# Kernel tuning notes

Measured on AMD Instinct MI355X. Metric: run time of the kernel, lower is better.

Reference implementation:

```python
import jax, jax.numpy as jnp
import numpy as np

B, T, J, D = 32, 2048, 256, 256


def setup_inputs() -> dict:
    key = jax.random.key(0)
    k1, k2, k3, k4, k5 = jax.random.split(key, 5)
    U = jax.random.normal(k1, (B, J, D), jnp.float32)
    H = jax.random.normal(k2, (B, T, D), jnp.float32)
    # realistic length-based binary masks (at least half the positions valid)
    u_len = jax.random.randint(k3, (B,), J // 2, J + 1)
    h_len = jax.random.randint(k4, (B,), T // 2, T + 1)
    U_mask = (jnp.arange(J)[None, :] < u_len[:, None]).astype(jnp.float32)
    H_mask = (jnp.arange(T)[None, :] < h_len[:, None]).astype(jnp.float32)
    # similarity_layer = nn.Linear(3*D, 1); bias initialized to 1.0 in __init__
    w = jax.random.normal(k5, (3 * D,), jnp.float32) * 0.02
    bias = jnp.ones((), jnp.float32)
    return {"U": U, "H": H, "U_mask": U_mask, "H_mask": H_mask, "w": w, "bias": bias}


def _masked_softmax(vector, mask):
    # softmax(vector * mask) * mask, renormalized along the softmax axis
    result = jax.nn.softmax(vector * mask, axis=-1) * mask
    return result / (jnp.sum(result, axis=-1, keepdims=True) + 1e-13)


def reference(U, H, U_mask, H_mask, w, bias):
    # Linear on cat([H, U, H*U]) decomposes into three terms; avoids the
    # (B, T, J, 3D) intermediate while computing identical math.
    w_h, w_u, w_hu = w[:D], w[D:2 * D], w[2 * D:]
    S = ((H @ w_h)[:, :, None]                      # (B, T, 1)
         + (U @ w_u)[:, None, :]                    # (B, 1, J)
         + jnp.einsum('btd,bjd->btj', H * w_hu, U)  # (B, T, J)
         + bias)

    # context-to-question attention: masked softmax over J, then bmm with U
    attn = _masked_softmax(S, U_mask[:, None, :])   # (B, T, J)
    c2q = jnp.einsum('btj,bjd->btd', attn, U)       # (B, T, D)

    # question-to-context: replace masked with -1e7, max over J, softmax over T
    um = U_mask[:, None, :]
    masked_sim = S * um + (-10000000.0) * (1.0 - um)
    mb = jnp.max(masked_sim, axis=-1)               # (B, T)
    b = _masked_softmax(mb, H_mask)                 # (B, T)
    q2c = jnp.einsum('bt,btd->bd', b, H)            # (B, D)

    G = jnp.concatenate([H, c2q, H * c2q, H * q2c[:, None, :]], axis=-1)  # (B, T, 4D)
    return (G, c2q, q2c)
```

## Files before the change

### kernel.cpp

```cpp
#include <hip/hip_runtime.h>
#include <hip/hip_bf16.h>

#define BB 32
#define TT 2048
#define JJ 256
#define DD 256

typedef __attribute__((ext_vector_type(4))) float f32x4;
typedef __attribute__((ext_vector_type(8))) short bf16x8;
typedef __attribute__((ext_vector_type(2))) unsigned int u32x2v;

static __device__ __forceinline__ unsigned short f2bf(float x) {
    unsigned u = __builtin_bit_cast(unsigned, x);
    u = (u + 0x7fffu + ((u >> 16) & 1u)) >> 16;
    return (unsigned short)u;
}
static __device__ __forceinline__ unsigned pack2(float a, float b) {
    return (unsigned)f2bf(a) | ((unsigned)f2bf(b) << 16);
}

static __device__ __forceinline__ void stage_slice(
    const unsigned short* __restrict__ Bsrc, char* pool, int buf, int kt, int tid, int wid)
{
    #pragma unroll
    for (int it = 0; it < 4; ++it) {
        int s = it * 256 + tid;
        int row = s >> 2, cp = s & 3;
        int c = cp ^ (row & 3);
        const char* src = (const char*)Bsrc + row * 512 + kt * 64 + c * 16;
        __builtin_amdgcn_global_load_lds(
            (const __attribute__((address_space(1))) unsigned int*)src,
            (__attribute__((address_space(3))) unsigned int*)(pool + (buf << 14) + (it << 12) + (wid << 10)),
            16, 0, 0);
    }
}

__global__ __launch_bounds__(256) void p0_prep(
    const float* __restrict__ U, const float* __restrict__ w,
    unsigned short* __restrict__ Ubf, unsigned short* __restrict__ UbfT,
    float* __restrict__ Uw, float* __restrict__ q2c_out)
{
    const int b = blockIdx.x >> 2, jc = blockIdx.x & 3;
    const int tid = threadIdx.x;
    if (jc == 0) q2c_out[b * 256 + tid] = 0.f;
    __shared__ unsigned short lt[64][258];
    const f32x4* U4 = (const f32x4*)U;
    const f32x4* W4 = (const f32x4*)w;
    for (int it = 0; it < 16; ++it) {
        int fi = it * 256 + tid;
        int lr = fi >> 6, c4 = fi & 63;
        int j = b * 256 + jc * 64 + lr;
        f32x4 u4 = U4[j * 64 + c4];
        unsigned short s0 = f2bf(u4[0]), s1 = f2bf(u4[1]), s2 = f2bf(u4[2]), s3 = f2bf(u4[3]);
        u32x2v pk; pk[0] = (unsigned)s0 | ((unsigned)s1 << 16); pk[1] = (unsigned)s2 | ((unsigned)s3 << 16);
        *(u32x2v*)(Ubf + j * 256 + c4 * 4) = pk;
        lt[lr][c4*4+0] = s0; lt[lr][c4*4+1] = s1; lt[lr][c4*4+2] = s2; lt[lr][c4*4+3] = s3;
        f32x4 wu = W4[64 + c4];
        float p = u4[0]*wu[0] + u4[1]*wu[1] + u4[2]*wu[2] + u4[3]*wu[3];
        #pragma unroll
        for (int o = 32; o; o >>= 1) p += __shfl_xor(p, o);
        if ((tid & 63) == 0) Uw[j] = p;
    }
    __syncthreads();
    for (int it2 = 0; it2 < 64; ++it2) {
        int d = it2 * 4 + (tid >> 6);
        int jl = tid & 63;
        UbfT[(b * 256 + d) * 256 + jc * 64 + jl] = lt[jl][d];
    }
}

__global__ __launch_bounds__(256, 3) void p1_main(
    const float* __restrict__ H, const float* __restrict__ Um,
    const float* __restrict__ w, const float* __restrict__ biasp,
    const unsigned short* __restrict__ Ubf, const unsigned short* __restrict__ UbfT,
    const float* __restrict__ Uw,
    float* __restrict__ mb, float* __restrict__ Gout, float* __restrict__ c2q_out)
{
    const int id = blockIdx.x;
    const int n = ((id & 7) << 7) | (id >> 3);
    const int b = n >> 5, tb = n & 31;
    const int t0 = tb * 64;
    const int tid = threadIdx.x;
    const int wid = tid >> 6, lane = tid & 63, g = lane >> 4, l16 = lane & 15;

    __shared__ __align__(16) char pool[36864];
    __shared__ float uw_lds[256];
    __shared__ float um_lds[256];
    __shared__ float rt_lds[64];

    const f32x4* H4 = (const f32x4*)H;
    const f32x4* W4 = (const f32x4*)w;
    f32x4* G4 = (f32x4*)Gout;
    f32x4* C2Q4 = (f32x4*)c2q_out;
    const float bias = biasp[0];
    const unsigned short* Ubf_b  = Ubf  + (size_t)b * 65536;
    const unsigned short* UbfT_b = UbfT + (size_t)b * 65536;

    uw_lds[tid] = Uw[b * 256 + tid];
    um_lds[tid] = Um[b * 256 + tid];

    for (int it = 0; it < 16; ++it) {
        int fi = it * 256 + tid;
        int lr = fi >> 6, c4 = fi & 63;
        f32x4 h4 = H4[(b * TT + t0 + lr) * 64 + c4];
        f32x4 whu = W4[128 + c4];
        f32x4 wh = W4[c4];
        G4[(b * TT + t0 + lr) * 256 + c4] = h4;
        f32x4 hw = h4 * whu;
        u32x2v pk; pk[0] = pack2(hw[0], hw[1]); pk[1] = pack2(hw[2], hw[3]);
        unsigned off = ((unsigned)(lr * 512 + c4 * 8)) ^ ((unsigned)((lr & 7) << 4));
        *(u32x2v*)(pool + off) = pk;
        float p = h4[0]*wh[0] + h4[1]*wh[1] + h4[2]*wh[2] + h4[3]*wh[3];
        #pragma unroll
        for (int o = 32; o; o >>= 1) p += __shfl_xor(p, o);
        if (lane == 0) rt_lds[lr] = p;
    }
    __syncthreads();

    bf16x8 af[8];
    {
        const int row = wid * 16 + l16;
        #pragma unroll
        for (int kt = 0; kt < 8; ++kt) {
            unsigned off = ((unsigned)(row * 512 + kt * 64 + g * 16)) ^ ((unsigned)((row & 7) << 4));
            af[kt] = *(const bf16x8*)(pool + off);
        }
    }
    __syncthreads();

    f32x4 acc[16];
    #pragma unroll
    for (int nt = 0; nt < 16; ++nt) acc[nt] = (f32x4)(0.0f);
    stage_slice(Ubf_b, pool, 0, 0, tid, wid);
    __syncthreads();
    #pragma unroll
    for (int kt = 0; kt < 8; ++kt) {
        if (kt < 7) stage_slice(Ubf_b, pool, (kt + 1) & 1, kt + 1, tid, wid);
        const char* bufp = pool + ((kt & 1) << 14);
        #pragma unroll
        for (int nt = 0; nt < 16; ++nt) {
            const int row = nt * 16 + l16;
            bf16x8 bfr = *(const bf16x8*)(bufp + row * 64 + ((g ^ (row & 3)) << 4));
            acc[nt] = __builtin_amdgcn_mfma_f32_16x16x32_bf16(af[kt], bfr, acc[nt], 0, 0, 0);
        }
        __syncthreads();
    }

    float rmax[4] = {-3e38f, -3e38f, -3e38f, -3e38f};
    #pragma unroll
    for (int nt = 0; nt < 16; ++nt) {
        float ct = uw_lds[nt * 16 + l16];
        float msk = um_lds[nt * 16 + l16];
        #pragma unroll
        for (int r = 0; r < 4; ++r) {
            float v = acc[nt][r] + ct;
            acc[nt][r] = v;
            if (msk > 0.5f) rmax[r] = fmaxf(rmax[r], v);
        }
    }
    #pragma unroll
    for (int r = 0; r < 4; ++r) {
        #pragma unroll
        for (int o = 1; o < 16; o <<= 1) rmax[r] = fmaxf(rmax[r], __shfl_xor(rmax[r], o));
    }
    float rsum[4] = {0.f, 0.f, 0.f, 0.f};
    #pragma unroll
    for (int nt = 0; nt < 16; ++nt) {
        float msk = um_lds[nt * 16 + l16];
        #pragma unroll
        for (int r = 0; r < 4; ++r) {
            float e = (msk > 0.5f) ? exp2f((acc[nt][r] - rmax[r]) * 1.44269504f) : 0.0f;
            acc[nt][r] = e;
            rsum[r] += e;
        }
    }
    #pragma unroll
    for (int r = 0; r < 4; ++r) {
        #pragma unroll
        for (int o = 1; o < 16; o <<= 1) rsum[r] += __shfl_xor(rsum[r], o);
    }
    if (l16 == 0) {
        #pragma unroll
        for (int r = 0; r < 4; ++r) {
            int lrow = wid * 16 + g * 4 + r;
            mb[b * TT + t0 + lrow] = rmax[r] + rt_lds[lrow] + bias;
        }
    }
    float inv[4];
    #pragma unroll
    for (int r = 0; r < 4; ++r) inv[r] = 1.0f / rsum[r];

    const unsigned wb = (unsigned)wid * 9216u;
    #pragma unroll
    for (int nt = 0; nt < 16; ++nt) {
        int j = nt * 16 + l16;
        unsigned lo = pack2(acc[nt][0] * inv[0], acc[nt][1] * inv[1]);
        unsigned hi = pack2(acc[nt][2] * inv[2], acc[nt][3] * inv[3]);
        char* p = pool + wb + (unsigned)(j * 36) + (unsigned)(g * 8);
        *(unsigned*)(p) = lo;
        *(unsigned*)(p + 4) = hi;
    }
    bf16x8 pa[8];
    #pragma unroll
    for (int kt = 0; kt < 8; ++kt) {
        #pragma unroll
        for (int jj = 0; jj < 8; ++jj) {
            int j = kt * 32 + g * 8 + jj;
            unsigned short pv = *(const unsigned short*)(pool + wb + (unsigned)(j * 36) + (unsigned)(l16 * 2));
            pa[kt][jj] = (short)pv;
        }
    }
    __syncthreads();

    f32x4 acc2[16];
    #pragma unroll
    for (int nt = 0; nt < 16; ++nt) acc2[nt] = (f32x4)(0.0f);
    stage_slice(UbfT_b, pool, 0, 0, tid, wid);
    __syncthreads();
    #pragma unroll
    for (int kt = 0; kt < 8; ++kt) {
        if (kt < 7) stage_slice(UbfT_b, pool, (kt + 1) & 1, kt + 1, tid, wid);
        const char* bufp = pool + ((kt & 1) << 14);
        #pragma unroll
        for (int nt = 0; nt < 16; ++nt) {
            const int row = nt * 16 + l16;
            bf16x8 bfr = *(const bf16x8*)(bufp + row * 64 + ((g ^ (row & 3)) << 4));
            acc2[nt] = __builtin_amdgcn_mfma_f32_16x16x32_bf16(pa[kt], bfr, acc2[nt], 0, 0, 0);
        }
        __syncthreads();
    }

    {
        float* lds_f = (float*)pool;
        const int c_ = lane & 31, rh = lane >> 5;
        #pragma unroll
        for (int half = 0; half < 2; ++half) {
            #pragma unroll
            for (int nt8 = 0; nt8 < 8; ++nt8) {
                int nt = half * 8 + nt8;
                int dcol = nt8 * 16 + l16;
                #pragma unroll
                for (int r = 0; r < 4; ++r) {
                    int row = wid * 16 + g * 4 + r;
                    lds_f[row * 132 + dcol] = acc2[nt][r];
                }
            }
            #pragma unroll
            for (int it3 = 0; it3 < 8; ++it3) {
                int row = wid * 16 + it3 * 2 + rh;
                f32x4 v = *(const f32x4*)&lds_f[row * 132 + c_ * 4];
                int t = t0 + row;
                f32x4 h4 = H4[(b * TT + t) * 64 + half * 32 + c_];
                int gb4 = (b * TT + t) * 256;
                G4[gb4 + 64 + half * 32 + c_] = v;
                G4[gb4 + 128 + half * 32 + c_] = h4 * v;
                C2Q4[(b * TT + t) * 64 + half * 32 + c_] = v;
            }
        }
    }
}

__global__ __launch_bounds__(256) void p2_fused(
    const float* __restrict__ mb, const float* __restrict__ Hm,
    const float* __restrict__ H, float* __restrict__ q2c_out)
{
    const int b = blockIdx.x >> 4, ch = blockIdx.x & 15;
    const int tid = threadIdx.x;
    __shared__ float red[8];
    float mv[8], hm[8];
    float lmax = -3e38f;
    #pragma unroll
    for (int k = 0; k < 8; ++k) {
        int t = k * 256 + tid;
        mv[k] = mb[b * TT + t];
        hm[k] = Hm[b * TT + t];
        if (hm[k] > 0.5f) lmax = fmaxf(lmax, mv[k]);
    }
    #pragma unroll
    for (int o = 32; o; o >>= 1) lmax = fmaxf(lmax, __shfl_xor(lmax, o));
    int wv = tid >> 6;
    if ((tid & 63) == 0) red[wv] = lmax;
    __syncthreads();
    lmax = fmaxf(fmaxf(red[0], red[1]), fmaxf(red[2], red[3]));
    float ls = 0.f;
    #pragma unroll
    for (int k = 0; k < 8; ++k)
        ls += (hm[k] > 0.5f) ? exp2f((mv[k] - lmax) * 1.44269504f) : 0.f;
    #pragma unroll
    for (int o = 32; o; o >>= 1) ls += __shfl_xor(ls, o);
    if ((tid & 63) == 0) red[4 + wv] = ls;
    __syncthreads();
    const float invs = 1.0f / (red[4] + red[5] + red[6] + red[7] + 1e-13f);

    const int tq = tid >> 6, dq = tid & 63;
    const f32x4* H4 = (const f32x4*)H;
    f32x4 a = (f32x4)(0.0f);
    for (int tt = tq; tt < 128; tt += 4) {
        int t = ch * 128 + tt;
        int k = t >> 8;
        (void)k;
        float bm = mb[b * TT + t];
        float hmv = Hm[b * TT + t];
        float bv = (hmv > 0.5f) ? exp2f((bm - lmax) * 1.44269504f) * invs : 0.f;
        a += bv * H4[(b * TT + t) * 64 + dq];
    }
    __shared__ f32x4 red4[4][64];
    red4[tq][dq] = a;
    __syncthreads();
    if (tid < 64) {
        f32x4 s = red4[0][tid] + red4[1][tid] + red4[2][tid] + red4[3][tid];
        #pragma unroll
        for (int c = 0; c < 4; ++c) atomicAdd(&q2c_out[b * 256 + tid * 4 + c], s[c]);
    }
}

__global__ __launch_bounds__(256) void p3_g3(
    const float* __restrict__ H, const float* __restrict__ q2c,
    float* __restrict__ Gout)
{
    int idx = blockIdx.x * 256 + threadIdx.x;
    int rowid = idx >> 6, c4 = idx & 63;
    int b = rowid >> 11;
    const f32x4* H4 = (const f32x4*)H;
    const f32x4* Q4 = (const f32x4*)q2c;
    f32x4* G4 = (f32x4*)Gout;
    f32x4 h4 = H4[idx];
    f32x4 q4 = Q4[b * 64 + c4];
    G4[rowid * 256 + 192 + c4] = h4 * q4;
}

extern "C" void kernel_launch(void* const* d_in, const int* in_sizes, int n_in,
                              void* d_out, int out_size, void* d_ws, size_t ws_size,
                              hipStream_t stream) {
    (void)in_sizes; (void)n_in; (void)out_size; (void)ws_size;
    const float* U    = (const float*)d_in[0];
    const float* H    = (const float*)d_in[1];
    const float* Um   = (const float*)d_in[2];
    const float* Hm   = (const float*)d_in[3];
    const float* w    = (const float*)d_in[4];
    const float* bias = (const float*)d_in[5];

    float* G   = (float*)d_out;
    float* c2q = G + (size_t)BB * TT * 1024;
    float* q2c = c2q + (size_t)BB * TT * 256;

    char* ws = (char*)d_ws;
    unsigned short* Ubf  = (unsigned short*)ws;
    unsigned short* UbfT = (unsigned short*)(ws + (4u << 20));
    float* Uw   = (float*)(ws + (8u << 20));
    float* mb   = (float*)(ws + (8u << 20) + (64u << 10));

    p0_prep<<<dim3(128), dim3(256), 0, stream>>>(U, w, Ubf, UbfT, Uw, q2c);
    p1_main<<<dim3(1024), dim3(256), 0, stream>>>(H, Um, w, bias, Ubf, UbfT, Uw, mb, G, c2q);
    p2_fused<<<dim3(512), dim3(256), 0, stream>>>(mb, Hm, H, q2c);
    p3_g3<<<dim3(16384), dim3(256), 0, stream>>>(H, q2c, G);
}
```

Before: 154.4 us.

## Use nontemporal stores, drop LDS transpose epilogue, batch p3 loads per thread

Output writes to G and c2q now use nontemporal stores so the large write stream bypasses cache retention. The p1 epilogue no longer transposes the MFMA accumulators through LDS and instead writes scalar elements straight from the accumulator layout. That saves the LDS round trip but gives narrower, strided global stores (16 contiguous floats per row group) and scalar H reloads. p3 now processes four vectors per thread with a quarter of the blocks, so more loads are in flight per thread.

New measurement: 187.2 us. 21.2% more time.

```diff
diff --git a/kernel.cpp b/kernel.cpp
--- a/kernel.cpp
+++ b/kernel.cpp
@@ -91,7 +91,6 @@
     const f32x4* H4 = (const f32x4*)H;
     const f32x4* W4 = (const f32x4*)w;
     f32x4* G4 = (f32x4*)Gout;
-    f32x4* C2Q4 = (f32x4*)c2q_out;
     const float bias = biasp[0];
     const unsigned short* Ubf_b  = Ubf  + (size_t)b * 65536;
     const unsigned short* UbfT_b = UbfT + (size_t)b * 65536;
@@ -105,7 +104,7 @@
         f32x4 h4 = H4[(b * TT + t0 + lr) * 64 + c4];
         f32x4 whu = W4[128 + c4];
         f32x4 wh = W4[c4];
-        G4[(b * TT + t0 + lr) * 256 + c4] = h4;
+        __builtin_nontemporal_store(h4, &G4[(b * TT + t0 + lr) * 256 + c4]);
         f32x4 hw = h4 * whu;
         u32x2v pk; pk[0] = pack2(hw[0], hw[1]); pk[1] = pack2(hw[2], hw[3]);
         unsigned off = ((unsigned)(lr * 512 + c4 * 8)) ^ ((unsigned)((lr & 7) << 4));
@@ -230,32 +229,18 @@
         __syncthreads();
     }
 
-    {
-        float* lds_f = (float*)pool;
-        const int c_ = lane & 31, rh = lane >> 5;
-        #pragma unroll
-        for (int half = 0; half < 2; ++half) {
-            #pragma unroll
-            for (int nt8 = 0; nt8 < 8; ++nt8) {
-                int nt = half * 8 + nt8;
-                int dcol = nt8 * 16 + l16;
-                #pragma unroll
-                for (int r = 0; r < 4; ++r) {
-                    int row = wid * 16 + g * 4 + r;
-                    lds_f[row * 132 + dcol] = acc2[nt][r];
-                }
-            }
-            #pragma unroll
-            for (int it3 = 0; it3 < 8; ++it3) {
-                int row = wid * 16 + it3 * 2 + rh;
-                f32x4 v = *(const f32x4*)&lds_f[row * 132 + c_ * 4];
-                int t = t0 + row;
-                f32x4 h4 = H4[(b * TT + t) * 64 + half * 32 + c_];
-                int gb4 = (b * TT + t) * 256;
-                G4[gb4 + 64 + half * 32 + c_] = v;
-                G4[gb4 + 128 + half * 32 + c_] = h4 * v;
-                C2Q4[(b * TT + t) * 64 + half * 32 + c_] = v;
-            }
+    #pragma unroll
+    for (int nt = 0; nt < 16; ++nt) {
+        int d = nt * 16 + l16;
+        #pragma unroll
+        for (int r = 0; r < 4; ++r) {
+            int t = t0 + wid * 16 + g * 4 + r;
+            float c = acc2[nt][r];
+            float h = H[(b * TT + t) * 256 + d];
+            int gbase = (b * TT + t) * 1024;
+            __builtin_nontemporal_store(c, &Gout[gbase + 256 + d]);
+            __builtin_nontemporal_store(h * c, &Gout[gbase + 512 + d]);
+            __builtin_nontemporal_store(c, &c2q_out[(b * TT + t) * 256 + d]);
         }
     }
 }
@@ -297,8 +282,6 @@
     f32x4 a = (f32x4)(0.0f);
     for (int tt = tq; tt < 128; tt += 4) {
         int t = ch * 128 + tt;
-        int k = t >> 8;
-        (void)k;
         float bm = mb[b * TT + t];
         float hmv = Hm[b * TT + t];
         float bv = (hmv > 0.5f) ? exp2f((bm - lmax) * 1.44269504f) * invs : 0.f;
@@ -318,15 +301,24 @@
     const float* __restrict__ H, const float* __restrict__ q2c,
     float* __restrict__ Gout)
 {
-    int idx = blockIdx.x * 256 + threadIdx.x;
-    int rowid = idx >> 6, c4 = idx & 63;
-    int b = rowid >> 11;
+    const int base = blockIdx.x * 1024 + threadIdx.x;
     const f32x4* H4 = (const f32x4*)H;
     const f32x4* Q4 = (const f32x4*)q2c;
     f32x4* G4 = (f32x4*)Gout;
-    f32x4 h4 = H4[idx];
-    f32x4 q4 = Q4[b * 64 + c4];
-    G4[rowid * 256 + 192 + c4] = h4 * q4;
+    f32x4 h[4];
+    int rowid[4], c4[4];
+    #pragma unroll
+    for (int k = 0; k < 4; ++k) {
+        int idx = base + k * 256;
+        rowid[k] = idx >> 6; c4[k] = idx & 63;
+        h[k] = __builtin_nontemporal_load(&H4[idx]);
+    }
+    #pragma unroll
+    for (int k = 0; k < 4; ++k) {
+        int b = rowid[k] >> 11;
+        f32x4 q4 = Q4[b * 64 + c4[k]];
+        __builtin_nontemporal_store(h[k] * q4, &G4[rowid[k] * 256 + 192 + c4[k]]);
+    }
 }
 
 extern "C" void kernel_launch(void* const* d_in, const int* in_sizes, int n_in,
@@ -353,5 +345,5 @@
     p0_prep<<<dim3(128), dim3(256), 0, stream>>>(U, w, Ubf, UbfT, Uw, q2c);
     p1_main<<<dim3(1024), dim3(256), 0, stream>>>(H, Um, w, bias, Ubf, UbfT, Uw, mb, G, c2q);
     p2_fused<<<dim3(512), dim3(256), 0, stream>>>(mb, Hm, H, q2c);
-    p3_g3<<<dim3(16384), dim3(256), 0, stream>>>(H, q2c, G);
-}
+    p3_g3<<<dim3(4096), dim3(256), 0, stream>>>(H, q2c, G);
+}
```

## Change LDS swizzle for B tiles and replace LDS-transpose epilogue with lane shuffles

Applied to the files above, without the earlier changes.

The XOR swizzle for staged U slices now uses (row>>1)&3 instead of row&3, aiming to cut LDS bank conflicts on the bf16x8 fragment reads. The c2q epilogue no longer round-trips the accumulator through LDS. It pairs adjacent lanes with __shfl_xor so each lane writes 2-float vectors directly to G, H*c2q and c2q. This removes the LDS stores, loads and barrier-free staging, but the global stores narrow from 16-byte to 8-byte accesses, which may hurt write coalescing efficiency.

Measured after the change: 152.3 us. Within noise of the previous version (-1.4%).

```diff
diff --git a/kernel.cpp b/kernel.cpp
--- a/kernel.cpp
+++ b/kernel.cpp
@@ -7,6 +7,7 @@
 #define DD 256
 
 typedef __attribute__((ext_vector_type(4))) float f32x4;
+typedef __attribute__((ext_vector_type(2))) float f32x2;
 typedef __attribute__((ext_vector_type(8))) short bf16x8;
 typedef __attribute__((ext_vector_type(2))) unsigned int u32x2v;
 
@@ -26,7 +27,7 @@
     for (int it = 0; it < 4; ++it) {
         int s = it * 256 + tid;
         int row = s >> 2, cp = s & 3;
-        int c = cp ^ (row & 3);
+        int c = cp ^ ((row >> 1) & 3);
         const char* src = (const char*)Bsrc + row * 512 + kt * 64 + c * 16;
         __builtin_amdgcn_global_load_lds(
             (const __attribute__((address_space(1))) unsigned int*)src,
@@ -91,7 +92,6 @@
     const f32x4* H4 = (const f32x4*)H;
     const f32x4* W4 = (const f32x4*)w;
     f32x4* G4 = (f32x4*)Gout;
-    f32x4* C2Q4 = (f32x4*)c2q_out;
     const float bias = biasp[0];
     const unsigned short* Ubf_b  = Ubf  + (size_t)b * 65536;
     const unsigned short* UbfT_b = UbfT + (size_t)b * 65536;
@@ -140,7 +140,7 @@
         #pragma unroll
         for (int nt = 0; nt < 16; ++nt) {
             const int row = nt * 16 + l16;
-            bf16x8 bfr = *(const bf16x8*)(bufp + row * 64 + ((g ^ (row & 3)) << 4));
+            bf16x8 bfr = *(const bf16x8*)(bufp + row * 64 + ((g ^ ((row >> 1) & 3)) << 4));
             acc[nt] = __builtin_amdgcn_mfma_f32_16x16x32_bf16(af[kt], bfr, acc[nt], 0, 0, 0);
         }
         __syncthreads();
@@ -224,37 +224,35 @@
         #pragma unroll
         for (int nt = 0; nt < 16; ++nt) {
             const int row = nt * 16 + l16;
-            bf16x8 bfr = *(const bf16x8*)(bufp + row * 64 + ((g ^ (row & 3)) << 4));
+            bf16x8 bfr = *(const bf16x8*)(bufp + row * 64 + ((g ^ ((row >> 1) & 3)) << 4));
             acc2[nt] = __builtin_amdgcn_mfma_f32_16x16x32_bf16(pa[kt], bfr, acc2[nt], 0, 0, 0);
         }
         __syncthreads();
     }
 
     {
-        float* lds_f = (float*)pool;
-        const int c_ = lane & 31, rh = lane >> 5;
-        #pragma unroll
-        for (int half = 0; half < 2; ++half) {
+        const bool odd = (l16 & 1) != 0;
+        #pragma unroll
+        for (int m = 0; m < 8; ++m) {
+            const int dA = (2 * m) * 16 + l16;
+            const int dB = (2 * m + 1) * 16 + l16 - 1;
+            const int d0 = odd ? dB : dA;
             #pragma unroll
-            for (int nt8 = 0; nt8 < 8; ++nt8) {
-                int nt = half * 8 + nt8;
-                int dcol = nt8 * 16 + l16;
-                #pragma unroll
-                for (int r = 0; r < 4; ++r) {
-                    int row = wid * 16 + g * 4 + r;
-                    lds_f[row * 132 + dcol] = acc2[nt][r];
-                }
-            }
-            #pragma unroll
-            for (int it3 = 0; it3 < 8; ++it3) {
-                int row = wid * 16 + it3 * 2 + rh;
-                f32x4 v = *(const f32x4*)&lds_f[row * 132 + c_ * 4];
-                int t = t0 + row;
-                f32x4 h4 = H4[(b * TT + t) * 64 + half * 32 + c_];
-                int gb4 = (b * TT + t) * 256;
-                G4[gb4 + 64 + half * 32 + c_] = v;
-                G4[gb4 + 128 + half * 32 + c_] = h4 * v;
-                C2Q4[(b * TT + t) * 64 + half * 32 + c_] = v;
+            for (int r = 0; r < 4; ++r) {
+                float cA = acc2[2 * m][r];
+                float cB = acc2[2 * m + 1][r];
+                float sA = __shfl_xor(cA, 1);
+                float sB = __shfl_xor(cB, 1);
+                f32x2 cp;
+                cp[0] = odd ? sB : cA;
+                cp[1] = odd ? cB : sA;
+                int t = t0 + wid * 16 + g * 4 + r;
+                const float* hrow = H + (b * TT + t) * 256;
+                f32x2 h2 = *(const f32x2*)(hrow + d0);
+                float* grow = Gout + (size_t)(b * TT + t) * 1024;
+                *(f32x2*)(grow + 256 + d0) = cp;
+                *(f32x2*)(grow + 512 + d0) = h2 * cp;
+                *(f32x2*)(c2q_out + (size_t)(b * TT + t) * 256 + d0) = cp;
             }
         }
     }
@@ -297,8 +295,6 @@
     f32x4 a = (f32x4)(0.0f);
     for (int tt = tq; tt < 128; tt += 4) {
         int t = ch * 128 + tt;
-        int k = t >> 8;
-        (void)k;
         float bm = mb[b * TT + t];
         float hmv = Hm[b * TT + t];
         float bv = (hmv > 0.5f) ? exp2f((bm - lmax) * 1.44269504f) * invs : 0.f;
```
